# Kernel optimization log

Hardware: AMD Instinct MI355X
Metric: run time of the kernel (lower is better)

The kernel has to match this reference:

```python
import jax, jax.numpy as jnp
import numpy as np

K1 = 3                      # spline kernel size per pseudo dim
SIZE = float(np.sqrt(2.0))  # pseudo_cartesian normalization size


def spline_weights(p, k):
    """Degree-1 open B-spline basis over 2D pseudo coords.
    p: [..., 2] in [0,1]. Returns basis [..., 4], weight_index [..., 4]."""
    v = jnp.clip(p, 0.0, 1.0) * (k - 1)
    lo = jnp.floor(v)
    frac = v - lo
    lo = lo.astype(jnp.int32)
    off = jnp.array([0, 1], dtype=jnp.int32)
    w0 = jnp.stack([1.0 - frac[..., 0], frac[..., 0]], axis=-1)   # [...,2]
    w1 = jnp.stack([1.0 - frac[..., 1], frac[..., 1]], axis=-1)   # [...,2]
    i0 = jnp.clip(lo[..., 0:1] + off, 0, k - 1)                    # [...,2]
    i1 = jnp.clip(lo[..., 1:2] + off, 0, k - 1)                    # [...,2]
    basis = (w0[..., :, None] * w1[..., None, :]).reshape(*p.shape[:-1], 4)
    widx = (i0[..., :, None] + k * i1[..., None, :]).reshape(*p.shape[:-1], 4)
    return basis, widx


def setup_inputs() -> dict:
    key = jax.random.key(0)
    kx, ke, kp, kq, kw, kb = jax.random.split(key, 6)
    N, C, P, E, K = 50000, 64, 16, 800000, K1 * K1
    x = jax.random.normal(kx, (N, C), dtype=jnp.float32)
    pos = jax.random.uniform(kp, (N, 2), dtype=jnp.float32)
    pose = jax.random.normal(kq, (N, P, 2), dtype=jnp.float32)
    pose = pose / (jnp.linalg.norm(pose, axis=-1, keepdims=True) + 1e-8)  # unit pose vectors
    W = jax.random.normal(kw, (P, K, C), dtype=jnp.float32) / np.sqrt(C * 4.0)
    bias = jax.random.normal(kb, (P,), dtype=jnp.float32) * 0.01
    edge_index = jax.random.randint(ke, (2, E), 0, N, dtype=jnp.int64)
    return {"x": x, "pos": pos, "pose": pose, "W": W, "bias": bias,
            "edge_index": edge_index}


def reference(x, pos, pose, W, bias, edge_index):
    N, C = x.shape
    P = pose.shape[1]
    row, col = edge_index[0], edge_index[1]
    # pseudo_cartesian: normalized relative position in [0,1]^2
    pseudo = (pos[col] - pos[row]) / (2.0 * SIZE) + 0.5              # [E,2]
    # posevec_to_rotmat on detached pose vectors
    pose_c = jax.lax.stop_gradient(pose)
    a, b = pose_c[..., 0], pose_c[..., 1]
    R = jnp.stack([jnp.stack([a, -b], -1), jnp.stack([b, a], -1)], -2)  # [N,P,2,2]
    Re = R[row]                                                      # [E,P,2,2]
    # rotate pseudo coords about (0.5, 0.5), batched over all poses
    p = jnp.einsum('epij,ej->epi', Re, pseudo - 0.5) + 0.5           # [E,P,2]
    basis, widx = spline_weights(p, K1)                              # [E,P,4]
    # SplineConv (out_channels=1, no root weight, no norm):
    # precompute per-node per-pose per-kernel-bin projections
    Z = jnp.einsum('nc,pkc->npk', x, W)                              # [N,P,K]
    pidx = jnp.arange(P)[None, :, None]
    vals = Z[col[:, None, None], pidx, widx]                         # [E,P,4]
    msg = jnp.sum(basis * vals, axis=-1)                             # [E,P]
    out = jax.ops.segment_sum(msg, row, num_segments=N)              # [N,P]
    return out + bias[None, :]
```

## Files before the change

### kernel.cpp

```cpp
#include <hip/hip_runtime.h>

#define C_DIM 64
#define P_DIM 16
#define K_DIM 9
#define PK (P_DIM * K_DIM)
#define INV2S 0.35355339059327373f

typedef __attribute__((ext_vector_type(8))) short short8v;
typedef __attribute__((ext_vector_type(4))) float f32x4;

__device__ __forceinline__ ushort f2bf(float f) {
    uint u = __builtin_bit_cast(uint, f);
    return (ushort)((u + 0x7FFFu + ((u >> 16) & 1u)) >> 16);
}
__device__ __forceinline__ float bf2f(ushort h) {
    return __builtin_bit_cast(float, ((uint)h) << 16);
}

#define ZSTRIDE 72

__global__ __launch_bounds__(256) void z_gemm_kernel(const float* __restrict__ x,
                                                     const float* __restrict__ W,
                                                     const float* __restrict__ bias,
                                                     const float* __restrict__ pose,
                                                     float* __restrict__ out,
                                                     ushort* __restrict__ Zb,
                                                     uint* __restrict__ pose_bf,
                                                     int N) {
    __shared__ ushort w_hi[PK * ZSTRIDE];
    __shared__ ushort w_lo[PK * ZSTRIDE];

    const int tid = threadIdx.x;
    const int block_row = blockIdx.x * 64;

    {
        const float4 b4 = ((const float4*)bias)[tid & 3];
        const int o4 = block_row * 4 + tid;
        if (o4 < N * 4) ((float4*)out)[o4] = b4;
    }

    if (pose_bf != nullptr) {
        for (int i = tid; i < 64 * P_DIM; i += 256) {
            const int r = block_row + (i >> 4);
            if (r < N) {
                const float2 ab = ((const float2*)pose)[(size_t)r * P_DIM + (i & 15)];
                pose_bf[(size_t)r * P_DIM + (i & 15)] =
                    (uint)f2bf(ab.x) | ((uint)f2bf(ab.y) << 16);
            }
        }
    }

    for (int i = tid; i < PK * (C_DIM / 2); i += 256) {
        const int n  = i >> 5;
        const int k2 = i & 31;
        const float2 w2 = ((const float2*)W)[i];
        const int o = n * ZSTRIDE + k2 * 2;
        const ushort h0 = f2bf(w2.x);
        const ushort h1 = f2bf(w2.y);
        w_hi[o]     = h0;
        w_hi[o + 1] = h1;
        w_lo[o]     = f2bf(w2.x - bf2f(h0));
        w_lo[o + 1] = f2bf(w2.y - bf2f(h1));
    }
    __syncthreads();

    const int lane = tid & 63;
    const int wv   = tid >> 6;
    const int col  = lane & 15;
    const int kg   = lane >> 4;

    const int arow = block_row + wv * 16 + col;
    const float* xr = x + (size_t)(arow < N ? arow : 0) * C_DIM;
    float4 x0 = ((const float4*)xr)[kg * 2];
    float4 x1 = ((const float4*)xr)[kg * 2 + 1];
    float4 x2 = ((const float4*)xr)[8 + kg * 2];
    float4 x3 = ((const float4*)xr)[8 + kg * 2 + 1];
    if (arow >= N) {
        x0 = x1 = x2 = x3 = make_float4(0.f, 0.f, 0.f, 0.f);
    }

    short8v a_hi0, a_lo0, a_hi1, a_lo1;
    {
        const float t0[8] = {x0.x, x0.y, x0.z, x0.w, x1.x, x1.y, x1.z, x1.w};
        const float t1[8] = {x2.x, x2.y, x2.z, x2.w, x3.x, x3.y, x3.z, x3.w};
        #pragma unroll
        for (int e = 0; e < 8; ++e) {
            const ushort h = f2bf(t0[e]);
            a_hi0[e] = (short)h;
            a_lo0[e] = (short)f2bf(t0[e] - bf2f(h));
            const ushort g = f2bf(t1[e]);
            a_hi1[e] = (short)g;
            a_lo1[e] = (short)f2bf(t1[e] - bf2f(g));
        }
    }

    const int orow0 = block_row + wv * 16 + kg * 4;

    #pragma unroll
    for (int nt = 0; nt < 9; ++nt) {
        const ushort* bhp = &w_hi[(nt * 16 + col) * ZSTRIDE + kg * 8];
        const ushort* blp = &w_lo[(nt * 16 + col) * ZSTRIDE + kg * 8];
        const short8v bh0 = *(const short8v*)bhp;
        const short8v bh1 = *(const short8v*)(bhp + 32);
        const short8v bl0 = *(const short8v*)blp;
        const short8v bl1 = *(const short8v*)(blp + 32);

        f32x4 acc = {0.f, 0.f, 0.f, 0.f};
        acc = __builtin_amdgcn_mfma_f32_16x16x32_bf16(a_lo0, bh0, acc, 0, 0, 0);
        acc = __builtin_amdgcn_mfma_f32_16x16x32_bf16(a_hi0, bl0, acc, 0, 0, 0);
        acc = __builtin_amdgcn_mfma_f32_16x16x32_bf16(a_lo1, bh1, acc, 0, 0, 0);
        acc = __builtin_amdgcn_mfma_f32_16x16x32_bf16(a_hi1, bl1, acc, 0, 0, 0);
        acc = __builtin_amdgcn_mfma_f32_16x16x32_bf16(a_hi0, bh0, acc, 0, 0, 0);
        acc = __builtin_amdgcn_mfma_f32_16x16x32_bf16(a_hi1, bh1, acc, 0, 0, 0);

        #pragma unroll
        for (int r = 0; r < 4; ++r) {
            const int row = orow0 + r;
            if (row < N) Zb[(size_t)row * PK + nt * 16 + col] = f2bf(acc[r]);
        }
    }
}

#define EILP 8
template <bool USEBF>
__global__ __launch_bounds__(256) void edge_kernel(const int* __restrict__ ei,
                                                   const float* __restrict__ pos,
                                                   const float* __restrict__ pose,
                                                   const uint* __restrict__ pose_bf,
                                                   const ushort* __restrict__ Zb,
                                                   float* __restrict__ out,
                                                   int E) {
    const int p  = threadIdx.x & 15;
    const int eg = threadIdx.x >> 4;
    const int e0 = blockIdx.x * (16 * EILP) + eg;

    int  r[EILP], c[EILP];
    bool valid[EILP];
    #pragma unroll
    for (int it = 0; it < EILP; ++it) {
        int e = e0 + it * 16;
        valid[it] = (e < E);
        int ec = valid[it] ? e : 0;
        r[it] = ei[ec];
        c[it] = ei[E + ec];
    }

    float d0[EILP], d1[EILP];
    #pragma unroll
    for (int it = 0; it < EILP; ++it) {
        const float2 pc = ((const float2*)pos)[c[it]];
        const float2 pr = ((const float2*)pos)[r[it]];
        d0[it] = (pc.x - pr.x) * INV2S;
        d1[it] = (pc.y - pr.y) * INV2S;
    }

    float a_[EILP], b_[EILP];
    #pragma unroll
    for (int it = 0; it < EILP; ++it) {
        if (USEBF) {
            const uint ab = pose_bf[(size_t)r[it] * P_DIM + p];
            a_[it] = bf2f((ushort)(ab & 0xffffu));
            b_[it] = bf2f((ushort)(ab >> 16));
        } else {
            const float2 ab = ((const float2*)pose)[(size_t)r[it] * P_DIM + p];
            a_[it] = ab.x;
            b_[it] = ab.y;
        }
    }

    #pragma unroll
    for (int it = 0; it < EILP; ++it) {
        const float p0 = fmaf(a_[it], d0[it], fmaf(-b_[it], d1[it], 0.5f));
        const float p1 = fmaf(b_[it], d0[it], fmaf( a_[it], d1[it], 0.5f));

        const float v0 = fminf(fmaxf(p0, 0.0f), 1.0f) * 2.0f;
        const float v1 = fminf(fmaxf(p1, 0.0f), 1.0f) * 2.0f;
        const float lo0 = floorf(v0);
        const float lo1 = floorf(v1);
        const float f0 = v0 - lo0;
        const float f1 = v1 - lo1;
        const int i00 = min((int)lo0, 2);
        const int i01 = min((int)lo0 + 1, 2);
        const int i10 = min((int)lo1, 2);
        const int i11 = min((int)lo1 + 1, 2);

        const ushort* __restrict__ Zp = Zb + (size_t)c[it] * PK + p * K_DIM;
        const float w00 = (1.0f - f0) * (1.0f - f1);
        const float w01 = (1.0f - f0) * f1;
        const float w10 = f0 * (1.0f - f1);
        const float w11 = f0 * f1;

        float m = w00 * bf2f(Zp[i00 + 3 * i10]);
        m = fmaf(w01, bf2f(Zp[i00 + 3 * i11]), m);
        m = fmaf(w10, bf2f(Zp[i01 + 3 * i10]), m);
        m = fmaf(w11, bf2f(Zp[i01 + 3 * i11]), m);

        if (valid[it]) atomicAdd(&out[(size_t)r[it] * P_DIM + p], m);
    }
}

extern "C" void kernel_launch(void* const* d_in, const int* in_sizes, int n_in,
                              void* d_out, int out_size, void* d_ws, size_t ws_size,
                              hipStream_t stream) {
    const float* x    = (const float*)d_in[0];
    const float* pos  = (const float*)d_in[1];
    const float* pose = (const float*)d_in[2];
    const float* W    = (const float*)d_in[3];
    const float* bias = (const float*)d_in[4];
    const int*   ei   = (const int*)d_in[5];

    const int N = in_sizes[0] / C_DIM;
    const int E = in_sizes[5] / 2;

    float* out = (float*)d_out;
    ushort* Zb = (ushort*)d_ws;

    const size_t zb_bytes   = (size_t)N * PK * sizeof(ushort);
    const size_t pose_bytes = (size_t)N * P_DIM * sizeof(uint);
    uint* pose_bf = (ws_size >= zb_bytes + pose_bytes)
                        ? (uint*)((char*)d_ws + zb_bytes) : nullptr;

    z_gemm_kernel<<<(N + 63) / 64, 256, 0, stream>>>(x, W, bias, pose, out, Zb, pose_bf, N);

    const int eblocks = (E + 16 * EILP - 1) / (16 * EILP);
    if (pose_bf != nullptr)
        edge_kernel<true><<<eblocks, 256, 0, stream>>>(ei, pos, pose, pose_bf, Zb, out, E);
    else
        edge_kernel<false><<<eblocks, 256, 0, stream>>>(ei, pos, pose, pose_bf, Zb, out, E);
}
```

Measured before the change: 144.7 us.

## Pad per-pose Z rows to ten entries and prefetch them as aligned words

The Z projection table is stored with each pose's 9 kernel-bin values padded to 10 bf16 entries. This lets every edge thread load its pose's entries as five aligned 32-bit words, issued up front for all edges in the batch. The four bilinear taps are then picked out with shifts and selects on the bin flags instead of doing four data-dependent 2-byte gathers after computing the spline indices. The aim is to remove the dependency between index computation and memory loads and to cut the number of load instructions. The cost is a slightly larger Z table and more registers held for the prefetched words.

After: 148.0 us. 1.02x slower.

```diff
diff --git a/kernel.cpp b/kernel.cpp
--- a/kernel.cpp
+++ b/kernel.cpp
@@ -3,7 +3,8 @@
 #define C_DIM 64
 #define P_DIM 16
 #define K_DIM 9
-#define PK (P_DIM * K_DIM)
+#define ZROW 10
+#define ZNODE (P_DIM * ZROW)
 #define INV2S 0.35355339059327373f
 
 typedef __attribute__((ext_vector_type(8))) short short8v;
@@ -27,8 +28,8 @@
                                                      ushort* __restrict__ Zb,
                                                      uint* __restrict__ pose_bf,
                                                      int N) {
-    __shared__ ushort w_hi[PK * ZSTRIDE];
-    __shared__ ushort w_lo[PK * ZSTRIDE];
+    __shared__ ushort w_hi[144 * ZSTRIDE];
+    __shared__ ushort w_lo[144 * ZSTRIDE];
 
     const int tid = threadIdx.x;
     const int block_row = blockIdx.x * 64;
@@ -50,7 +51,7 @@
         }
     }
 
-    for (int i = tid; i < PK * (C_DIM / 2); i += 256) {
+    for (int i = tid; i < 144 * (C_DIM / 2); i += 256) {
         const int n  = i >> 5;
         const int k2 = i & 31;
         const float2 w2 = ((const float2*)W)[i];
@@ -113,10 +114,12 @@
         acc = __builtin_amdgcn_mfma_f32_16x16x32_bf16(a_hi0, bh0, acc, 0, 0, 0);
         acc = __builtin_amdgcn_mfma_f32_16x16x32_bf16(a_hi1, bh1, acc, 0, 0, 0);
 
+        const int j  = nt * 16 + col;
+        const int zi = (j / 9) * ZROW + (j % 9);
         #pragma unroll
         for (int r = 0; r < 4; ++r) {
             const int row = orow0 + r;
-            if (row < N) Zb[(size_t)row * PK + nt * 16 + col] = f2bf(acc[r]);
+            if (row < N) Zb[(size_t)row * ZNODE + zi] = f2bf(acc[r]);
         }
     }
 }
@@ -168,6 +171,17 @@
         }
     }
 
+    uint q0[EILP], q1[EILP], q2[EILP], q3[EILP], q4[EILP];
+    #pragma unroll
+    for (int it = 0; it < EILP; ++it) {
+        const uint* Zp = (const uint*)(Zb + (size_t)c[it] * ZNODE) + p * (ZROW / 2);
+        q0[it] = Zp[0];
+        q1[it] = Zp[1];
+        q2[it] = Zp[2];
+        q3[it] = Zp[3];
+        q4[it] = Zp[4];
+    }
+
     #pragma unroll
     for (int it = 0; it < EILP; ++it) {
         const float p0 = fmaf(a_[it], d0[it], fmaf(-b_[it], d1[it], 0.5f));
@@ -175,25 +189,30 @@
 
         const float v0 = fminf(fmaxf(p0, 0.0f), 1.0f) * 2.0f;
         const float v1 = fminf(fmaxf(p1, 0.0f), 1.0f) * 2.0f;
-        const float lo0 = floorf(v0);
-        const float lo1 = floorf(v1);
-        const float f0 = v0 - lo0;
-        const float f1 = v1 - lo1;
-        const int i00 = min((int)lo0, 2);
-        const int i01 = min((int)lo0 + 1, 2);
-        const int i10 = min((int)lo1, 2);
-        const int i11 = min((int)lo1 + 1, 2);
-
-        const ushort* __restrict__ Zp = Zb + (size_t)c[it] * PK + p * K_DIM;
+        const bool b0 = (v0 >= 1.0f);
+        const bool b1 = (v1 >= 1.0f);
+        const float f0 = v0 - (b0 ? 1.0f : 0.0f);
+        const float f1 = v1 - (b1 ? 1.0f : 0.0f);
+
+        const uint A0 = q0[it], A1 = q1[it], A2 = q2[it], A3 = q3[it], A4 = q4[it];
+        const uint W0 = b1 ? ((A1 >> 16) | (A2 << 16)) : A0;
+        const uint W1 = b1 ? ((A2 >> 16) | (A3 << 16)) : A1;
+        const uint W2 = b1 ? ((A3 >> 16) | (A4 << 16)) : A2;
+        const uint s = b0 ? 16u : 0u;
+        const float z00 = bf2f((ushort)(W0 >> s));
+        const float z10 = bf2f((ushort)(b0 ? (W1 & 0xffffu) : (W0 >> 16)));
+        const float z01 = bf2f((ushort)(b0 ? (W2 & 0xffffu) : (W1 >> 16)));
+        const float z11 = bf2f((ushort)(W2 >> s));
+
         const float w00 = (1.0f - f0) * (1.0f - f1);
         const float w01 = (1.0f - f0) * f1;
         const float w10 = f0 * (1.0f - f1);
         const float w11 = f0 * f1;
 
-        float m = w00 * bf2f(Zp[i00 + 3 * i10]);
-        m = fmaf(w01, bf2f(Zp[i00 + 3 * i11]), m);
-        m = fmaf(w10, bf2f(Zp[i01 + 3 * i10]), m);
-        m = fmaf(w11, bf2f(Zp[i01 + 3 * i11]), m);
+        float m = w00 * z00;
+        m = fmaf(w01, z01, m);
+        m = fmaf(w10, z10, m);
+        m = fmaf(w11, z11, m);
 
         if (valid[it]) atomicAdd(&out[(size_t)r[it] * P_DIM + p], m);
     }
@@ -215,7 +234,7 @@
     float* out = (float*)d_out;
     ushort* Zb = (ushort*)d_ws;
 
-    const size_t zb_bytes   = (size_t)N * PK * sizeof(ushort);
+    const size_t zb_bytes   = (size_t)N * ZNODE * sizeof(ushort);
     const size_t pose_bytes = (size_t)N * P_DIM * sizeof(uint);
     uint* pose_bf = (ws_size >= zb_bytes + pose_bytes)
                         ? (uint*)((char*)d_ws + zb_bytes) : nullptr;
```
